# Performance work log

Hardware: AMD Instinct MI355X
Metric: run time of the kernel (lower is better)

The kernel has to match this reference:

```python
import jax, jax.numpy as jnp
from jax import lax
import numpy as np

K = 1024      # kernel_size
S = 256       # stride
CUT = 513     # kernel_size//2 + 1
TC = 2 * CUT  # transform_channels = 1026
CH = 8        # combine_hidden
B = 32
TIME = 262144


def setup_inputs() -> dict:
    key = jax.random.key(0)
    ks = jax.random.split(key, 12)
    x = jax.random.normal(ks[0], (B, 1, TIME), dtype=jnp.float32)
    conv1_w = jax.random.normal(ks[1], (TC, 1, K), dtype=jnp.float32) * 0.02
    in_gamma = 1.0 + 0.1 * jax.random.normal(ks[2], (TC,), dtype=jnp.float32)
    comb1_w = jax.random.normal(ks[3], (CH, 2), dtype=jnp.float32) * 0.5
    comb1_b = jax.random.normal(ks[4], (CH,), dtype=jnp.float32) * 0.1
    comb2_w = jax.random.normal(ks[5], (1, CH), dtype=jnp.float32) * 0.5
    comb2_b = jax.random.normal(ks[6], (1,), dtype=jnp.float32) * 0.1
    lin_w = jax.random.normal(ks[7], (CUT, CUT), dtype=jnp.float32) * 0.04
    lin_b = jax.random.normal(ks[8], (CUT,), dtype=jnp.float32) * 0.02
    fc_gamma = 1.0 + 0.1 * jax.random.normal(ks[9], (CUT,), dtype=jnp.float32)
    convT_w = jax.random.normal(ks[10], (TC, 2, K), dtype=jnp.float32) * 0.02  # torch ConvTranspose1d (Cin, Cout, K)
    return {"x": x, "conv1_w": conv1_w, "in_gamma": in_gamma,
            "comb1_w": comb1_w, "comb1_b": comb1_b,
            "comb2_w": comb2_w, "comb2_b": comb2_b,
            "lin_w": lin_w, "lin_b": lin_b, "fc_gamma": fc_gamma,
            "convT_w": convT_w}


def reference(x, conv1_w, in_gamma, comb1_w, comb1_b, comb2_w, comb2_b,
              lin_w, lin_b, fc_gamma, convT_w):
    time = x.shape[2]
    # conv1: Conv1d(1, TC, K, stride=S, padding=K), no bias
    t = lax.conv_general_dilated(x, conv1_w, window_strides=(S,),
                                 padding=[(K, K)],
                                 dimension_numbers=("NCH", "OIH", "NCH"))
    # ConvScaler1d (per-channel scale) + tanh activation
    t = jnp.tanh(t * in_gamma[None, :, None])  # (B, TC, F)
    real_x, imag_x = t[:, :CUT, :], t[:, CUT:, :]
    spec = jnp.stack([real_x, imag_x], axis=1)  # (B, 2, CUT, F)
    # combine1/combine2: 1x1 Conv2d + relu
    h = jax.nn.relu(jnp.einsum("bcxf,oc->boxf", spec, comb1_w)
                    + comb1_b[None, :, None, None])
    h = jax.nn.relu(jnp.einsum("bcxf,oc->boxf", h, comb2_w)
                    + comb2_b[None, :, None, None])[:, 0]  # (B, CUT, F)
    # FC over frequency axis per (batch, frame)
    hh = h.transpose(0, 2, 1)  # (B, F, CUT)
    hh = (hh @ lin_w.T + lin_b) * fc_gamma  # BitwiseLinear + Scaler
    mask = (jnp.tanh(hh) + 1.0) * 0.5       # output_transform -> [0,1]
    mask = mask.transpose(0, 2, 1)          # (B, CUT, F)
    mask = jnp.concatenate([mask, mask], axis=1)  # (B, TC, F)
    t = t * mask
    # conv1_transpose: ConvTranspose1d(TC, 2, K, stride=S), no bias
    wt = jnp.flip(convT_w.transpose(1, 0, 2), axis=2)  # (2, TC, K) flipped
    y = lax.conv_general_dilated(t, wt, window_strides=(1,),
                                 padding=[(K - 1, K - 1)],
                                 lhs_dilation=(S,),
                                 dimension_numbers=("NCH", "OIH", "NCH"))
    y = y[:, :, K:time + K]  # (B, 2, time)
    return jax.nn.softmax(y, axis=1)
```

## Files before the change

### kernel.cpp

```cpp
#include <hip/hip_runtime.h>
#include <cstddef>
#include <cstdint>

#define TIME_N 262144
#define BATCH  32
#define KW     1024
#define ST     256
#define CUTN   513
#define TCN    1026
#define FN     1029
#define FPAD   1152
#define CPAD   1152
#define XLEN   (FPAD * ST + KW)
#define XBLK   (XLEN / 256)

#define MROWS  (BATCH * FN)
#define MP     33024
#define KPH    544
#define NPH    640
#define TBP    1040
#define FLATB  (FN * TBP)
#define KPC    4160

#define PB_XPAD  (XBLK * BATCH)
#define PB_WBF   (PB_XPAD + CPAD)
#define PB_WLIN  (PB_WBF + NPH)
#define PB_TOTAL (PB_WLIN + KPC)

typedef __bf16 bf16x8 __attribute__((ext_vector_type(8)));
typedef float floatx4 __attribute__((ext_vector_type(4)));
typedef int   intx4   __attribute__((ext_vector_type(4)));

__device__ __forceinline__ unsigned short f2bf(float f) {
    union { float f; unsigned u; } v; v.f = f;
    unsigned r = (v.u + 0x7fffu + ((v.u >> 16) & 1u)) >> 16;
    return (unsigned short)r;
}
__device__ __forceinline__ float bf2f(unsigned short s) {
    union { unsigned u; float f; } v; v.u = ((unsigned)s) << 16;
    return v.f;
}
__device__ __forceinline__ int permch(int n) {
    return (n & 1) ? (CUTN + (n >> 1)) : (n >> 1);
}

__device__ __forceinline__ void load_lds16(const void* g, void* l) {
    __builtin_amdgcn_global_load_lds(
        (const __attribute__((address_space(1))) void*)g,
        (__attribute__((address_space(3))) void*)l, 16, 0, 0);
}

__global__ __launch_bounds__(256) void k_prep(
    const float* __restrict__ x, const float* __restrict__ c1w,
    const float* __restrict__ lw, const float* __restrict__ wct,
    unsigned short* __restrict__ xb, unsigned short* __restrict__ wbf,
    unsigned short* __restrict__ wlb, unsigned short* __restrict__ wdb)
{
    const int bid = blockIdx.x;
    if (bid < PB_XPAD) {
        const int b = bid / XBLK;
        const int p = (bid - b * XBLK) * 256 + threadIdx.x;
        const int g = p - KW;
        float v = (g >= 0 && g < TIME_N) ? x[(size_t)b * TIME_N + g] : 0.0f;
        xb[(size_t)b * XLEN + p] = f2bf(v);
    } else if (bid < PB_WBF) {
        const int n = bid - PB_XPAD;
        const int ch = (n < TCN) ? permch(n) : 0;
        for (int k = threadIdx.x; k < KW; k += 256) {
            float v = (n < TCN) ? c1w[(size_t)ch * KW + k] : 0.0f;
            wbf[(size_t)n * KW + k] = f2bf(v);
        }
    } else if (bid < PB_WLIN) {
        const int n = bid - PB_WBF;
        for (int k = threadIdx.x; k < KPH; k += 256) {
            float v = (n < CUTN && k < CUTN) ? lw[(size_t)n * CUTN + k] : 0.0f;
            wlb[(size_t)n * KPH + k] = f2bf(v);
        }
    } else {
        const int k = bid - PB_WLIN;
        const int r = threadIdx.x;
        const int j = k / TBP;
        const int n = k - j * TBP;
        float v = 0.0f;
        if (n < TCN) {
            const int ch = permch(n);
            const int widx = (3 - j) * 256 + r;
            v = wct[(size_t)(2 * ch) * KW + widx] -
                wct[(size_t)(2 * ch + 1) * KW + widx];
        }
        wdb[(size_t)r * KPC + k] = f2bf(v);
    }
}

__global__ __launch_bounds__(256) void k_conv1m(
    const unsigned short* __restrict__ xb, const unsigned short* __restrict__ wb,
    const float* __restrict__ gamma,
    const float* __restrict__ c1w, const float* __restrict__ c1b,
    const float* __restrict__ c2w, const float* __restrict__ c2b,
    unsigned short* __restrict__ tb2, unsigned short* __restrict__ h)
{
    extern __shared__ __align__(16) char lds[];

    const int flat = blockIdx.x;
    const int xcd = flat & 7;
    const int idx = flat >> 3;
    const int cb  = idx % 9;
    const int pr  = xcd * 36 + idx / 9;
    const int b   = pr / 9;
    const int fb  = pr % 9;
    const int f0 = fb * 128, c0 = cb * 128;
    const int tid = threadIdx.x;

    const unsigned short* xrow = xb + (size_t)b * XLEN;
    const unsigned short* ga[2];
    const unsigned short* gb[2];
    int qa[2];
#pragma unroll
    for (int i = 0; i < 2; ++i) {
        const int c = i * 256 + tid;
        const int row = c >> 2;
        const int colb = (c & 3) * 16;
        const int es = (colb ^ (((row >> 1) & 3) << 4)) >> 1;
        qa[i] = c * 16;
        ga[i] = xrow + (size_t)(f0 + row) * ST + es;
        gb[i] = wb + (size_t)(c0 + row) * KW + es;
    }

    const int wave = tid >> 6, lane = tid & 63;
    const int lm = lane & 15, lq = lane >> 4;
    const int mw = (wave & 1) * 64, nw = (wave >> 1) * 64;
    const int swz = ((lm >> 1) & 3) << 4;
    const int abo = (mw + lm) * 64 + ((lq * 16) ^ swz);
    const int bbo = 8192 + (nw + lm) * 64 + ((lq * 16) ^ swz);

    floatx4 acc[4][4];
#pragma unroll
    for (int i = 0; i < 4; ++i)
#pragma unroll
        for (int j = 0; j < 4; ++j) acc[i][j] = (floatx4)0.0f;

#pragma unroll
    for (int i = 0; i < 2; ++i) {
        load_lds16(ga[i], lds + qa[i]);
        load_lds16(gb[i], lds + 8192 + qa[i]);
        ga[i] += 32; gb[i] += 32;
    }

    for (int t = 0; t < KW / 32 - 1; ++t) {
        char* cur = lds + (t & 1) * 16384;
        char* nxt = lds + ((t + 1) & 1) * 16384;

#pragma unroll
        for (int i = 0; i < 2; ++i) {
            load_lds16(ga[i], nxt + qa[i]);
            load_lds16(gb[i], nxt + 8192 + qa[i]);
            ga[i] += 32; gb[i] += 32;
        }
        asm volatile("s_waitcnt vmcnt(4)" ::: "memory");
        __builtin_amdgcn_sched_barrier(0);
        __builtin_amdgcn_s_barrier();

        bf16x8 afr[4], bfr[4];
#pragma unroll
        for (int mt = 0; mt < 4; ++mt)
            afr[mt] = *(const bf16x8*)(cur + abo + mt * 1024);
#pragma unroll
        for (int nt = 0; nt < 4; ++nt)
            bfr[nt] = *(const bf16x8*)(cur + bbo + nt * 1024);
        asm volatile("s_waitcnt lgkmcnt(0)" ::: "memory");
        __builtin_amdgcn_sched_barrier(0);
        __builtin_amdgcn_s_barrier();

        __builtin_amdgcn_s_setprio(1);
#pragma unroll
        for (int mt = 0; mt < 4; ++mt)
#pragma unroll
            for (int nt = 0; nt < 4; ++nt)
                acc[mt][nt] = __builtin_amdgcn_mfma_f32_16x16x32_bf16(
                    afr[mt], bfr[nt], acc[mt][nt], 0, 0, 0);
        __builtin_amdgcn_s_setprio(0);
    }
    {
        char* cur = lds + ((KW / 32 - 1) & 1) * 16384;
        asm volatile("s_waitcnt vmcnt(0)" ::: "memory");
        __builtin_amdgcn_sched_barrier(0);
        __builtin_amdgcn_s_barrier();

        bf16x8 afr[4], bfr[4];
#pragma unroll
        for (int mt = 0; mt < 4; ++mt)
            afr[mt] = *(const bf16x8*)(cur + abo + mt * 1024);
#pragma unroll
        for (int nt = 0; nt < 4; ++nt)
            bfr[nt] = *(const bf16x8*)(cur + bbo + nt * 1024);
#pragma unroll
        for (int mt = 0; mt < 4; ++mt)
#pragma unroll
            for (int nt = 0; nt < 4; ++nt)
                acc[mt][nt] = __builtin_amdgcn_mfma_f32_16x16x32_bf16(
                    afr[mt], bfr[nt], acc[mt][nt], 0, 0, 0);
    }
    __syncthreads();

    float w1[16], b1[8], w2[8];
#pragma unroll
    for (int o = 0; o < 8; ++o) {
        w1[2 * o]     = c1w[2 * o];
        w1[2 * o + 1] = c1w[2 * o + 1];
        b1[o] = c1b[o];
        w2[o] = c2w[o];
    }
    const float b2v = c2b[0];
    const bool evenlane = ((lane & 1) == 0);

#pragma unroll
    for (int nt = 0; nt < 4; ++nt) {
        const int nl = nw + nt * 16 + lm;
        const int n = c0 + nl;
        const bool valid_c = (n < TCN);
        const float gv = valid_c ? gamma[permch(n)] : 0.0f;
        const int nbl = nl & ~1;
        const int yl  = nl >> 1;
#pragma unroll
        for (int mt = 0; mt < 4; ++mt) {
#pragma unroll
            for (int rp = 0; rp < 2; ++rp) {
                const int ra = rp * 2;
                const int fl = mw + mt * 16 + lq * 4 + ra;
                const float ua = acc[mt][nt][ra] * gv;
                const float ub = acc[mt][nt][ra + 1] * gv;
                const float ta  = 2.0f / (1.0f + __expf(-2.0f * ua)) - 1.0f;
                const float tbv = 2.0f / (1.0f + __expf(-2.0f * ub)) - 1.0f;
                const float sa = __shfl_xor(ta, 1);
                const float sb = __shfl_xor(tbv, 1);
                const int  fme = evenlane ? fl : (fl + 1);
                const float re = evenlane ? ta : sb;
                const float im = evenlane ? sa : tbv;
                const unsigned pr2 = (unsigned)f2bf(re) |
                                     ((unsigned)f2bf(im) << 16);
                *(unsigned*)(lds + fme * 256 + nbl * 2) = pr2;
                float a2 = b2v;
#pragma unroll
                for (int o = 0; o < 8; ++o) {
                    const float a1 = fmaxf(
                        re * w1[2 * o] + im * w1[2 * o + 1] + b1[o], 0.0f);
                    a2 += a1 * w2[o];
                }
                *(unsigned short*)(lds + 32768 + fme * 128 + yl * 2) =
                    f2bf(fmaxf(a2, 0.0f));
            }
        }
    }
    __syncthreads();

    const int vch = min(16, max(0, (520 - (c0 >> 1)) >> 2));
    unsigned short* tbb = tb2 + (size_t)b * FLATB;
#pragma unroll
    for (int i = 0; i < 8; ++i) {
        const int c = i * 256 + tid;
        const int fl = c >> 4;
        const int c16 = c & 15;
        if (f0 + fl < FN && c16 < vch) {
            const intx4 v = *(const intx4*)(lds + c * 16);
            *(intx4*)(tbb + (size_t)(f0 + fl) * TBP + (c0 + c16 * 8)) = v;
        }
    }
    const int vhc = min(8, max(0, (544 - (c0 >> 1)) >> 3));
#pragma unroll
    for (int i = 0; i < 4; ++i) {
        const int c = i * 256 + tid;
        const int fl = c >> 3;
        const int c16 = c & 7;
        if (f0 + fl < FN && c16 < vhc) {
            const intx4 v = *(const intx4*)(lds + 32768 + c * 16);
            *(intx4*)(h + ((size_t)b * FN + f0 + fl) * KPH +
                      ((c0 >> 1) + c16 * 8)) = v;
        }
    }
}

__global__ __launch_bounds__(256) void k_maskm(
    const unsigned short* __restrict__ h, const unsigned short* __restrict__ wlb,
    const float* __restrict__ linb, const float* __restrict__ fcg,
    unsigned* __restrict__ tbu)
{
    __shared__ __align__(16) unsigned short As[128 * 32];
    __shared__ __align__(16) unsigned short Bs[128 * 32];

    const int m0 = blockIdx.x * 128, n0 = blockIdx.y * 128;
    const int tid = threadIdx.x;

    const int s0 = tid, s1 = tid + 256;
    const int ar0 = s0 >> 2, aq0 = s0 & 3;
    const int ar1 = s1 >> 2, aq1 = s1 & 3;
    const unsigned short* ga0 = h + (size_t)(m0 + ar0) * KPH + aq0 * 8;
    const unsigned short* ga1 = h + (size_t)(m0 + ar1) * KPH + aq1 * 8;
    const unsigned short* gb0 = wlb + (size_t)(n0 + ar0) * KPH + aq0 * 8;
    const unsigned short* gb1 = wlb + (size_t)(n0 + ar1) * KPH + aq1 * 8;
    unsigned short* la0 = &As[s0 * 8];
    unsigned short* la1 = &As[s1 * 8];
    unsigned short* lb0 = &Bs[s0 * 8];
    unsigned short* lb1 = &Bs[s1 * 8];

    const int wave = tid >> 6, lane = tid & 63;
    const int lm = lane & 15, lq = lane >> 4;
    const int mw = (wave & 1) * 64, nw = (wave >> 1) * 64;
    const unsigned short* Ap = &As[(mw + lm) * 32 + lq * 8];
    const unsigned short* Bp = &Bs[(nw + lm) * 32 + lq * 8];

    floatx4 acc[4][4];
#pragma unroll
    for (int i = 0; i < 4; ++i)
#pragma unroll
        for (int j = 0; j < 4; ++j) acc[i][j] = (floatx4)0.0f;

    for (int ks = 0; ks < KPH / 32; ++ks) {
        load_lds16(ga0, la0);
        load_lds16(ga1, la1);
        load_lds16(gb0, lb0);
        load_lds16(gb1, lb1);
        ga0 += 32; ga1 += 32; gb0 += 32; gb1 += 32;
        __syncthreads();

        bf16x8 afr[4], bfr[4];
#pragma unroll
        for (int mt = 0; mt < 4; ++mt) afr[mt] = *(const bf16x8*)(Ap + mt * 16 * 32);
#pragma unroll
        for (int nt = 0; nt < 4; ++nt) bfr[nt] = *(const bf16x8*)(Bp + nt * 16 * 32);
#pragma unroll
        for (int mt = 0; mt < 4; ++mt)
#pragma unroll
            for (int nt = 0; nt < 4; ++nt)
                acc[mt][nt] = __builtin_amdgcn_mfma_f32_16x16x32_bf16(
                    afr[mt], bfr[nt], acc[mt][nt], 0, 0, 0);
        __syncthreads();
    }

#pragma unroll
    for (int nt = 0; nt < 4; ++nt) {
        const int y = n0 + nw + nt * 16 + lm;
        if (y < CUTN) {
            const float lb = linb[y];
            const float gv = fcg[y];
#pragma unroll
            for (int mt = 0; mt < 4; ++mt) {
#pragma unroll
                for (int r = 0; r < 4; ++r) {
                    const int m = m0 + mw + mt * 16 + lq * 4 + r;
                    if (m < MROWS) {
                        const float v = (acc[mt][nt][r] + lb) * gv;
                        const float msk = 1.0f / (1.0f + __expf(-2.0f * v));
                        unsigned* p = tbu + (size_t)m * (TBP / 2) + y;
                        const unsigned u = *p;
                        const float re = bf2f((unsigned short)(u & 0xffffu)) * msk;
                        const float im = bf2f((unsigned short)(u >> 16)) * msk;
                        *p = (unsigned)f2bf(re) | ((unsigned)f2bf(im) << 16);
                    }
                }
            }
        }
    }
}

__global__ __launch_bounds__(256) void k_convtm(
    const unsigned short* __restrict__ tb2, const unsigned short* __restrict__ wdb,
    float* __restrict__ out)
{
    extern __shared__ __align__(16) char lds[];

    const int m0 = blockIdx.x * 128, n0 = blockIdx.y * 128;
    const int b   = m0 >> 10;
    const int ml0 = m0 & 1023;
    const int tid = threadIdx.x;

    const unsigned short* tbb = tb2 + (size_t)b * FLATB;
    const unsigned short* ga[4];
    const unsigned short* gb[4];
    int qa[4];
#pragma unroll
    for (int i = 0; i < 4; ++i) {
        const int c = i * 256 + tid;
        const int row = c >> 3;
        const int colb = (c & 7) * 16;
        const int es = (colb ^ ((row & 7) << 4)) >> 1;
        qa[i] = c * 16;
        ga[i] = tbb + (size_t)(ml0 + row + 1) * TBP + es;
        gb[i] = wdb + (size_t)(n0 + row) * KPC + es;
    }

    const int wave = tid >> 6, lane = tid & 63;
    const int lm = lane & 15, lq = lane >> 4;
    const int mw = (wave & 1) * 64, nw = (wave >> 1) * 64;
    const int swz = (lm & 7) << 4;
    int abo[2], bbo[2];
#pragma unroll
    for (int ks = 0; ks < 2; ++ks) {
        abo[ks] = (mw + lm) * 128 + ((ks * 64 + lq * 16) ^ swz);
        bbo[ks] = 16384 + (nw + lm) * 128 + ((ks * 64 + lq * 16) ^ swz);
    }

    floatx4 acc[4][4];
#pragma unroll
    for (int i = 0; i < 4; ++i)
#pragma unroll
        for (int j = 0; j < 4; ++j) acc[i][j] = (floatx4)0.0f;

#pragma unroll
    for (int i = 0; i < 4; ++i) {
        load_lds16(ga[i], lds + qa[i]);
        load_lds16(gb[i], lds + 16384 + qa[i]);
        ga[i] += 64; gb[i] += 64;
    }
    __syncthreads();

    for (int t = 0; t < KPC / 64; ++t) {
        char* cur = lds + (t & 1) * 32768;
        char* nxt = lds + ((t + 1) & 1) * 32768;

        if (t + 1 < KPC / 64) {
#pragma unroll
            for (int i = 0; i < 4; ++i) {
                load_lds16(ga[i], nxt + qa[i]);
                load_lds16(gb[i], nxt + 16384 + qa[i]);
                ga[i] += 64; gb[i] += 64;
            }
        }

        bf16x8 afr[4][2], bfr[4][2];
#pragma unroll
        for (int mt = 0; mt < 4; ++mt)
#pragma unroll
            for (int ks = 0; ks < 2; ++ks)
                afr[mt][ks] = *(const bf16x8*)(cur + abo[ks] + mt * 2048);
#pragma unroll
        for (int nt = 0; nt < 4; ++nt)
#pragma unroll
            for (int ks = 0; ks < 2; ++ks)
                bfr[nt][ks] = *(const bf16x8*)(cur + bbo[ks] + nt * 2048);
#pragma unroll
        for (int mt = 0; mt < 4; ++mt)
#pragma unroll
            for (int nt = 0; nt < 4; ++nt)
#pragma unroll
                for (int ks = 0; ks < 2; ++ks)
                    acc[mt][nt] = __builtin_amdgcn_mfma_f32_16x16x32_bf16(
                        afr[mt][ks], bfr[nt][ks], acc[mt][nt], 0, 0, 0);
        __syncthreads();
    }

#pragma unroll
    for (int nt = 0; nt < 4; ++nt) {
        const int nl = nw + nt * 16 + lm;
#pragma unroll
        for (int mt = 0; mt < 4; ++mt) {
#pragma unroll
            for (int r = 0; r < 4; ++r) {
                const int ml = mw + mt * 16 + lq * 4 + r;
                const float d = acc[mt][nt][r];
                const float p0 = 1.0f / (1.0f + __expf(-d));
                *(float*)(lds + ml * 512 + nl * 4) = p0;
            }
        }
    }
    __syncthreads();

    float* ob = out + (size_t)b * 2 * TIME_N;
#pragma unroll
    for (int i = 0; i < 16; ++i) {
        const int c = i * 256 + tid;
        const int ml = c >> 5;
        const int c16 = c & 31;
        const floatx4 v = *(const floatx4*)(lds + c * 16);
        floatx4 w;
        w[0] = 1.0f - v[0]; w[1] = 1.0f - v[1];
        w[2] = 1.0f - v[2]; w[3] = 1.0f - v[3];
        const int tau = (ml0 + ml) * 256 + n0 + c16 * 4;
        *(floatx4*)(ob + tau)          = v;
        *(floatx4*)(ob + TIME_N + tau) = w;
    }
}

extern "C" void kernel_launch(void* const* d_in, const int* in_sizes, int n_in,
                              void* d_out, int out_size, void* d_ws, size_t ws_size,
                              hipStream_t stream)
{
    const float* x    = (const float*)d_in[0];
    const float* c1w  = (const float*)d_in[1];
    const float* ing  = (const float*)d_in[2];
    const float* cb1w = (const float*)d_in[3];
    const float* cb1b = (const float*)d_in[4];
    const float* cb2w = (const float*)d_in[5];
    const float* cb2b = (const float*)d_in[6];
    const float* linw = (const float*)d_in[7];
    const float* linb = (const float*)d_in[8];
    const float* fcg  = (const float*)d_in[9];
    const float* ctw  = (const float*)d_in[10];
    float* out = (float*)d_out;

    unsigned short* tb2 = (unsigned short*)d_ws;
    unsigned short* h   = tb2 + (size_t)BATCH * FLATB;
    unsigned short* wlb = h + (size_t)MP * KPH;
    unsigned short* xb  = wlb + (size_t)NPH * KPH;
    unsigned short* wbf = xb + (size_t)BATCH * XLEN;
    unsigned short* wdb = wbf + (size_t)CPAD * KW;

    hipLaunchKernelGGL(k_prep, dim3(PB_TOTAL), dim3(256), 0, stream,
                       x, c1w, linw, ctw, xb, wbf, wlb, wdb);
    hipLaunchKernelGGL(k_conv1m, dim3(BATCH * 9 * 9), dim3(256), 49152, stream,
                       xb, wbf, ing, cb1w, cb1b, cb2w, cb2b, tb2, h);
    hipLaunchKernelGGL(k_maskm, dim3(MP / 128, NPH / 128), dim3(256), 0, stream,
                       h, wlb, linb, fcg, (unsigned*)tb2);
    hipLaunchKernelGGL(k_convtm, dim3(256, 2), dim3(256), 65536, stream,
                       tb2, wdb, out);
}
```

Before: 445.7 us.

## Triple-buffer conv1 LDS pipeline, swizzle epilogue LDS, stage mask writes through LDS

The conv1 GEMM main loop moves from double to triple buffering, so two tiles of global-to-LDS loads stay in flight behind each compute step. Its epilogue LDS writes and reads get an XOR swizzle to cut bank conflicts. The mask GEMM epilogue now stages sigmoid values in shared memory and applies them with coalesced 16-byte read-modify-writes to tb, replacing scattered 4-byte accesses. The prep kernel's convT weight transform now uses one block per row with a loop, instead of one block per column, which gives coalesced writes. The cost is more LDS use, which may lower occupancy.

```diff
diff --git a/kernel.cpp b/kernel.cpp
--- a/kernel.cpp
+++ b/kernel.cpp
@@ -25,7 +25,7 @@
 #define PB_XPAD  (XBLK * BATCH)
 #define PB_WBF   (PB_XPAD + CPAD)
 #define PB_WLIN  (PB_WBF + NPH)
-#define PB_TOTAL (PB_WLIN + KPC)
+#define PB_TOTAL (PB_WLIN + 256)
 
 typedef __bf16 bf16x8 __attribute__((ext_vector_type(8)));
 typedef float floatx4 __attribute__((ext_vector_type(4)));
@@ -77,18 +77,20 @@
             wlb[(size_t)n * KPH + k] = f2bf(v);
         }
     } else {
-        const int k = bid - PB_WLIN;
-        const int r = threadIdx.x;
-        const int j = k / TBP;
-        const int n = k - j * TBP;
-        float v = 0.0f;
-        if (n < TCN) {
-            const int ch = permch(n);
-            const int widx = (3 - j) * 256 + r;
-            v = wct[(size_t)(2 * ch) * KW + widx] -
-                wct[(size_t)(2 * ch + 1) * KW + widx];
-        }
-        wdb[(size_t)r * KPC + k] = f2bf(v);
+        const int r = bid - PB_WLIN;
+        for (int k = threadIdx.x; k < KPC; k += 256) {
+            const int j = (k >= 3 * TBP) ? 3 : (k >= 2 * TBP) ? 2 :
+                          (k >= TBP) ? 1 : 0;
+            const int n = k - j * TBP;
+            float v = 0.0f;
+            if (n < TCN) {
+                const int ch = permch(n);
+                const int widx = (3 - j) * 256 + r;
+                v = wct[(size_t)(2 * ch) * KW + widx] -
+                    wct[(size_t)(2 * ch + 1) * KW + widx];
+            }
+            wdb[(size_t)r * KPC + k] = f2bf(v);
+        }
     }
 }
 
@@ -139,34 +141,41 @@
 #pragma unroll
         for (int j = 0; j < 4; ++j) acc[i][j] = (floatx4)0.0f;
 
+    char* bA = lds;
+    char* bB = lds + 16384;
+    char* bC = lds + 32768;
+
 #pragma unroll
     for (int i = 0; i < 2; ++i) {
-        load_lds16(ga[i], lds + qa[i]);
-        load_lds16(gb[i], lds + 8192 + qa[i]);
+        load_lds16(ga[i], bA + qa[i]);
+        load_lds16(gb[i], bA + 8192 + qa[i]);
         ga[i] += 32; gb[i] += 32;
     }
-
-    for (int t = 0; t < KW / 32 - 1; ++t) {
-        char* cur = lds + (t & 1) * 16384;
-        char* nxt = lds + ((t + 1) & 1) * 16384;
-
+#pragma unroll
+    for (int i = 0; i < 2; ++i) {
+        load_lds16(ga[i], bB + qa[i]);
+        load_lds16(gb[i], bB + 8192 + qa[i]);
+        ga[i] += 32; gb[i] += 32;
+    }
+
+    for (int t = 0; t < KW / 32 - 2; ++t) {
 #pragma unroll
         for (int i = 0; i < 2; ++i) {
-            load_lds16(ga[i], nxt + qa[i]);
-            load_lds16(gb[i], nxt + 8192 + qa[i]);
+            load_lds16(ga[i], bC + qa[i]);
+            load_lds16(gb[i], bC + 8192 + qa[i]);
             ga[i] += 32; gb[i] += 32;
         }
-        asm volatile("s_waitcnt vmcnt(4)" ::: "memory");
+        asm volatile("s_waitcnt vmcnt(8)" ::: "memory");
         __builtin_amdgcn_sched_barrier(0);
         __builtin_amdgcn_s_barrier();
 
         bf16x8 afr[4], bfr[4];
 #pragma unroll
         for (int mt = 0; mt < 4; ++mt)
-            afr[mt] = *(const bf16x8*)(cur + abo + mt * 1024);
+            afr[mt] = *(const bf16x8*)(bA + abo + mt * 1024);
 #pragma unroll
         for (int nt = 0; nt < 4; ++nt)
-            bfr[nt] = *(const bf16x8*)(cur + bbo + nt * 1024);
+            bfr[nt] = *(const bf16x8*)(bA + bbo + nt * 1024);
         asm volatile("s_waitcnt lgkmcnt(0)" ::: "memory");
         __builtin_amdgcn_sched_barrier(0);
         __builtin_amdgcn_s_barrier();
@@ -179,9 +188,32 @@
                 acc[mt][nt] = __builtin_amdgcn_mfma_f32_16x16x32_bf16(
                     afr[mt], bfr[nt], acc[mt][nt], 0, 0, 0);
         __builtin_amdgcn_s_setprio(0);
+
+        char* tmp = bA; bA = bB; bB = bC; bC = tmp;
     }
     {
-        char* cur = lds + ((KW / 32 - 1) & 1) * 16384;
+        asm volatile("s_waitcnt vmcnt(4)" ::: "memory");
+        __builtin_amdgcn_sched_barrier(0);
+        __builtin_amdgcn_s_barrier();
+
+        bf16x8 afr[4], bfr[4];
+#pragma unroll
+        for (int mt = 0; mt < 4; ++mt)
+            afr[mt] = *(const bf16x8*)(bA + abo + mt * 1024);
+#pragma unroll
+        for (int nt = 0; nt < 4; ++nt)
+            bfr[nt] = *(const bf16x8*)(bA + bbo + nt * 1024);
+        asm volatile("s_waitcnt lgkmcnt(0)" ::: "memory");
+        __builtin_amdgcn_sched_barrier(0);
+#pragma unroll
+        for (int mt = 0; mt < 4; ++mt)
+#pragma unroll
+            for (int nt = 0; nt < 4; ++nt)
+                acc[mt][nt] = __builtin_amdgcn_mfma_f32_16x16x32_bf16(
+                    afr[mt], bfr[nt], acc[mt][nt], 0, 0, 0);
+        char* tmp = bA; bA = bB; bB = bC; bC = tmp;
+    }
+    {
         asm volatile("s_waitcnt vmcnt(0)" ::: "memory");
         __builtin_amdgcn_sched_barrier(0);
         __builtin_amdgcn_s_barrier();
@@ -189,10 +221,12 @@
         bf16x8 afr[4], bfr[4];
 #pragma unroll
         for (int mt = 0; mt < 4; ++mt)
-            afr[mt] = *(const bf16x8*)(cur + abo + mt * 1024);
+            afr[mt] = *(const bf16x8*)(bA + abo + mt * 1024);
 #pragma unroll
         for (int nt = 0; nt < 4; ++nt)
-            bfr[nt] = *(const bf16x8*)(cur + bbo + nt * 1024);
+            bfr[nt] = *(const bf16x8*)(bA + bbo + nt * 1024);
+        asm volatile("s_waitcnt lgkmcnt(0)" ::: "memory");
+        __builtin_amdgcn_sched_barrier(0);
 #pragma unroll
         for (int mt = 0; mt < 4; ++mt)
 #pragma unroll
@@ -238,7 +272,8 @@
                 const float im = evenlane ? sa : tbv;
                 const unsigned pr2 = (unsigned)f2bf(re) |
                                      ((unsigned)f2bf(im) << 16);
-                *(unsigned*)(lds + fme * 256 + nbl * 2) = pr2;
+                const int xr = ((fme & 1) << 5) | (((fme >> 2) & 1) << 6);
+                *(unsigned*)(lds + fme * 256 + ((nbl * 2) ^ xr)) = pr2;
                 float a2 = b2v;
 #pragma unroll
                 for (int o = 0; o < 8; ++o) {
@@ -246,7 +281,8 @@
                         re * w1[2 * o] + im * w1[2 * o + 1] + b1[o], 0.0f);
                     a2 += a1 * w2[o];
                 }
-                *(unsigned short*)(lds + 32768 + fme * 128 + yl * 2) =
+                const int xh = ((fme & 1) << 4) | (((fme >> 2) & 1) << 5);
+                *(unsigned short*)(lds + 32768 + fme * 128 + ((yl * 2) ^ xh)) =
                     f2bf(fmaxf(a2, 0.0f));
             }
         }
@@ -261,7 +297,8 @@
         const int fl = c >> 4;
         const int c16 = c & 15;
         if (f0 + fl < FN && c16 < vch) {
-            const intx4 v = *(const intx4*)(lds + c * 16);
+            const int xr = ((fl & 1) << 5) | (((fl >> 2) & 1) << 6);
+            const intx4 v = *(const intx4*)(lds + fl * 256 + ((c16 * 16) ^ xr));
             *(intx4*)(tbb + (size_t)(f0 + fl) * TBP + (c0 + c16 * 8)) = v;
         }
     }
@@ -272,7 +309,9 @@
         const int fl = c >> 3;
         const int c16 = c & 7;
         if (f0 + fl < FN && c16 < vhc) {
-            const intx4 v = *(const intx4*)(lds + 32768 + c * 16);
+            const int xh = ((fl & 1) << 4) | (((fl >> 2) & 1) << 5);
+            const intx4 v = *(const intx4*)(lds + 32768 + fl * 128 +
+                                            ((c16 * 16) ^ xh));
             *(intx4*)(h + ((size_t)b * FN + f0 + fl) * KPH +
                       ((c0 >> 1) + c16 * 8)) = v;
         }
@@ -286,6 +325,7 @@
 {
     __shared__ __align__(16) unsigned short As[128 * 32];
     __shared__ __align__(16) unsigned short Bs[128 * 32];
+    __shared__ __align__(16) float stage[64][132];
 
     const int m0 = blockIdx.x * 128, n0 = blockIdx.y * 128;
     const int tid = threadIdx.x;
@@ -337,28 +377,63 @@
     }
 
 #pragma unroll
-    for (int nt = 0; nt < 4; ++nt) {
-        const int y = n0 + nw + nt * 16 + lm;
-        if (y < CUTN) {
-            const float lb = linb[y];
-            const float gv = fcg[y];
-#pragma unroll
-            for (int mt = 0; mt < 4; ++mt) {
-#pragma unroll
-                for (int r = 0; r < 4; ++r) {
-                    const int m = m0 + mw + mt * 16 + lq * 4 + r;
-                    if (m < MROWS) {
-                        const float v = (acc[mt][nt][r] + lb) * gv;
-                        const float msk = 1.0f / (1.0f + __expf(-2.0f * v));
-                        unsigned* p = tbu + (size_t)m * (TBP / 2) + y;
-                        const unsigned u = *p;
-                        const float re = bf2f((unsigned short)(u & 0xffffu)) * msk;
-                        const float im = bf2f((unsigned short)(u >> 16)) * msk;
-                        *p = (unsigned)f2bf(re) | ((unsigned)f2bf(im) << 16);
+    for (int pass = 0; pass < 2; ++pass) {
+        if ((wave & 1) == pass) {
+#pragma unroll
+            for (int nt = 0; nt < 4; ++nt) {
+                const int y = n0 + nw + nt * 16 + lm;
+                if (y < CUTN) {
+                    const float lb = linb[y];
+                    const float gv = fcg[y];
+#pragma unroll
+                    for (int mt = 0; mt < 4; ++mt)
+#pragma unroll
+                        for (int r = 0; r < 4; ++r) {
+                            const float v = (acc[mt][nt][r] + lb) * gv;
+                            stage[mt * 16 + lq * 4 + r][nw + nt * 16 + lm] =
+                                1.0f / (1.0f + __expf(-2.0f * v));
+                        }
+                }
+            }
+        }
+        __syncthreads();
+
+        const int base_m = m0 + pass * 64;
+        if (n0 + 128 <= CUTN) {
+#pragma unroll
+            for (int it = 0; it < 8; ++it) {
+                const int t2 = it * 256 + tid;
+                const int row = t2 >> 5, cc = t2 & 31;
+                const int m = base_m + row;
+                if (m < MROWS) {
+                    unsigned* p = tbu + (size_t)m * (TBP / 2) + n0 + cc * 4;
+                    const floatx4 mk = *(const floatx4*)&stage[row][cc * 4];
+                    intx4 uv = *(intx4*)p;
+#pragma unroll
+                    for (int j = 0; j < 4; ++j) {
+                        const unsigned u = (unsigned)uv[j];
+                        const float re = bf2f((unsigned short)(u & 0xffffu)) * mk[j];
+                        const float im = bf2f((unsigned short)(u >> 16)) * mk[j];
+                        uv[j] = (int)((unsigned)f2bf(re) |
+                                      ((unsigned)f2bf(im) << 16));
                     }
+                    *(intx4*)p = uv;
                 }
             }
-        }
+        } else {
+            if (tid < 64) {
+                const int m = base_m + tid;
+                if (m < MROWS) {
+                    unsigned* p = tbu + (size_t)m * (TBP / 2) + 512;
+                    const float mk = stage[tid][0];
+                    const unsigned u = *p;
+                    const float re = bf2f((unsigned short)(u & 0xffffu)) * mk;
+                    const float im = bf2f((unsigned short)(u >> 16)) * mk;
+                    *p = (unsigned)f2bf(re) | ((unsigned)f2bf(im) << 16);
+                }
+            }
+        }
+        __syncthreads();
     }
 }
 
```

Measured after the change: 476.0 us. +6.8%, slower.

## Load conv1 GEMM operands directly from global into registers, swizzle epilogue LDS

Applied to the files above, without the earlier changes.

The conv1 GEMM main loop drops the LDS double-buffered staging with barriers. Each wave now loads its MFMA fragments straight from global memory into registers, using a two-stage register ping-pong to overlap loads with MFMAs. The epilogue LDS staging writes and reads gain an XOR swizzle to reduce bank conflicts. The trade-off is that blocks no longer share operand tiles through LDS, so global/L2 traffic per block rises (each tile is read by two waves). It also removes barrier stalls and LDS round-trips.

```diff
diff --git a/kernel.cpp b/kernel.cpp
--- a/kernel.cpp
+++ b/kernel.cpp
@@ -111,27 +111,19 @@
     const int f0 = fb * 128, c0 = cb * 128;
     const int tid = threadIdx.x;
 
-    const unsigned short* xrow = xb + (size_t)b * XLEN;
-    const unsigned short* ga[2];
-    const unsigned short* gb[2];
-    int qa[2];
-#pragma unroll
-    for (int i = 0; i < 2; ++i) {
-        const int c = i * 256 + tid;
-        const int row = c >> 2;
-        const int colb = (c & 3) * 16;
-        const int es = (colb ^ (((row >> 1) & 3) << 4)) >> 1;
-        qa[i] = c * 16;
-        ga[i] = xrow + (size_t)(f0 + row) * ST + es;
-        gb[i] = wb + (size_t)(c0 + row) * KW + es;
-    }
-
     const int wave = tid >> 6, lane = tid & 63;
     const int lm = lane & 15, lq = lane >> 4;
     const int mw = (wave & 1) * 64, nw = (wave >> 1) * 64;
-    const int swz = ((lm >> 1) & 3) << 4;
-    const int abo = (mw + lm) * 64 + ((lq * 16) ^ swz);
-    const int bbo = 8192 + (nw + lm) * 64 + ((lq * 16) ^ swz);
+
+    const unsigned short* xrow = xb + (size_t)b * XLEN;
+    const unsigned short* pa[4];
+    const unsigned short* pb[4];
+#pragma unroll
+    for (int mt = 0; mt < 4; ++mt)
+        pa[mt] = xrow + (size_t)(f0 + mw + mt * 16 + lm) * ST + lq * 8;
+#pragma unroll
+    for (int nt = 0; nt < 4; ++nt)
+        pb[nt] = wb + (size_t)(c0 + nw + nt * 16 + lm) * KW + lq * 8;
 
     floatx4 acc[4][4];
 #pragma unroll
@@ -139,68 +131,34 @@
 #pragma unroll
         for (int j = 0; j < 4; ++j) acc[i][j] = (floatx4)0.0f;
 
-#pragma unroll
-    for (int i = 0; i < 2; ++i) {
-        load_lds16(ga[i], lds + qa[i]);
-        load_lds16(gb[i], lds + 8192 + qa[i]);
-        ga[i] += 32; gb[i] += 32;
-    }
-
-    for (int t = 0; t < KW / 32 - 1; ++t) {
-        char* cur = lds + (t & 1) * 16384;
-        char* nxt = lds + ((t + 1) & 1) * 16384;
-
-#pragma unroll
-        for (int i = 0; i < 2; ++i) {
-            load_lds16(ga[i], nxt + qa[i]);
-            load_lds16(gb[i], nxt + 8192 + qa[i]);
-            ga[i] += 32; gb[i] += 32;
-        }
-        asm volatile("s_waitcnt vmcnt(4)" ::: "memory");
-        __builtin_amdgcn_sched_barrier(0);
-        __builtin_amdgcn_s_barrier();
-
-        bf16x8 afr[4], bfr[4];
-#pragma unroll
-        for (int mt = 0; mt < 4; ++mt)
-            afr[mt] = *(const bf16x8*)(cur + abo + mt * 1024);
-#pragma unroll
-        for (int nt = 0; nt < 4; ++nt)
-            bfr[nt] = *(const bf16x8*)(cur + bbo + nt * 1024);
-        asm volatile("s_waitcnt lgkmcnt(0)" ::: "memory");
-        __builtin_amdgcn_sched_barrier(0);
-        __builtin_amdgcn_s_barrier();
-
-        __builtin_amdgcn_s_setprio(1);
+    bf16x8 aA[4], bA[4], aB[4], bB[4];
+#pragma unroll
+    for (int mt = 0; mt < 4; ++mt) { aA[mt] = *(const bf16x8*)pa[mt]; pa[mt] += 32; }
+#pragma unroll
+    for (int nt = 0; nt < 4; ++nt) { bA[nt] = *(const bf16x8*)pb[nt]; pb[nt] += 32; }
+
+    for (int t = 0; t < 16; ++t) {
+#pragma unroll
+        for (int mt = 0; mt < 4; ++mt) { aB[mt] = *(const bf16x8*)pa[mt]; pa[mt] += 32; }
+#pragma unroll
+        for (int nt = 0; nt < 4; ++nt) { bB[nt] = *(const bf16x8*)pb[nt]; pb[nt] += 32; }
 #pragma unroll
         for (int mt = 0; mt < 4; ++mt)
 #pragma unroll
             for (int nt = 0; nt < 4; ++nt)
                 acc[mt][nt] = __builtin_amdgcn_mfma_f32_16x16x32_bf16(
-                    afr[mt], bfr[nt], acc[mt][nt], 0, 0, 0);
-        __builtin_amdgcn_s_setprio(0);
-    }
-    {
-        char* cur = lds + ((KW / 32 - 1) & 1) * 16384;
-        asm volatile("s_waitcnt vmcnt(0)" ::: "memory");
-        __builtin_amdgcn_sched_barrier(0);
-        __builtin_amdgcn_s_barrier();
-
-        bf16x8 afr[4], bfr[4];
-#pragma unroll
-        for (int mt = 0; mt < 4; ++mt)
-            afr[mt] = *(const bf16x8*)(cur + abo + mt * 1024);
-#pragma unroll
-        for (int nt = 0; nt < 4; ++nt)
-            bfr[nt] = *(const bf16x8*)(cur + bbo + nt * 1024);
+                    aA[mt], bA[nt], acc[mt][nt], 0, 0, 0);
+#pragma unroll
+        for (int mt = 0; mt < 4; ++mt) { aA[mt] = *(const bf16x8*)pa[mt]; pa[mt] += 32; }
+#pragma unroll
+        for (int nt = 0; nt < 4; ++nt) { bA[nt] = *(const bf16x8*)pb[nt]; pb[nt] += 32; }
 #pragma unroll
         for (int mt = 0; mt < 4; ++mt)
 #pragma unroll
             for (int nt = 0; nt < 4; ++nt)
                 acc[mt][nt] = __builtin_amdgcn_mfma_f32_16x16x32_bf16(
-                    afr[mt], bfr[nt], acc[mt][nt], 0, 0, 0);
-    }
-    __syncthreads();
+                    aB[mt], bB[nt], acc[mt][nt], 0, 0, 0);
+    }
 
     float w1[16], b1[8], w2[8];
 #pragma unroll
@@ -238,7 +196,8 @@
                 const float im = evenlane ? sa : tbv;
                 const unsigned pr2 = (unsigned)f2bf(re) |
                                      ((unsigned)f2bf(im) << 16);
-                *(unsigned*)(lds + fme * 256 + nbl * 2) = pr2;
+                const int xr = ((fme & 1) << 5) | (((fme >> 2) & 1) << 6);
+                *(unsigned*)(lds + fme * 256 + ((nbl * 2) ^ xr)) = pr2;
                 float a2 = b2v;
 #pragma unroll
                 for (int o = 0; o < 8; ++o) {
@@ -246,7 +205,8 @@
                         re * w1[2 * o] + im * w1[2 * o + 1] + b1[o], 0.0f);
                     a2 += a1 * w2[o];
                 }
-                *(unsigned short*)(lds + 32768 + fme * 128 + yl * 2) =
+                const int xh = ((fme & 1) << 4) | (((fme >> 2) & 1) << 5);
+                *(unsigned short*)(lds + 32768 + fme * 128 + ((yl * 2) ^ xh)) =
                     f2bf(fmaxf(a2, 0.0f));
             }
         }
@@ -261,7 +221,8 @@
         const int fl = c >> 4;
         const int c16 = c & 15;
         if (f0 + fl < FN && c16 < vch) {
-            const intx4 v = *(const intx4*)(lds + c * 16);
+            const int xr = ((fl & 1) << 5) | (((fl >> 2) & 1) << 6);
+            const intx4 v = *(const intx4*)(lds + fl * 256 + ((c16 * 16) ^ xr));
             *(intx4*)(tbb + (size_t)(f0 + fl) * TBP + (c0 + c16 * 8)) = v;
         }
     }
@@ -272,7 +233,9 @@
         const int fl = c >> 3;
         const int c16 = c & 7;
         if (f0 + fl < FN && c16 < vhc) {
-            const intx4 v = *(const intx4*)(lds + 32768 + c * 16);
+            const int xh = ((fl & 1) << 4) | (((fl >> 2) & 1) << 5);
+            const intx4 v = *(const intx4*)(lds + 32768 + fl * 128 +
+                                            ((c16 * 16) ^ xh));
             *(intx4*)(h + ((size_t)b * FN + f0 + fl) * KPH +
                       ((c0 >> 1) + c16 * 8)) = v;
         }
```

After: 642.7 us. 44.2% more time.
